# Kernel tuning notes

Hardware: AMD Instinct MI355X
Metric: run time of the kernel (lower is better)

Reference implementation:

```python
import jax, jax.numpy as jnp
import numpy as np

D_MODEL = 1024
NUM_HEADS = 16
DILATION_RATES = [2, 2, 2]
SEGMENT_SIZES = [64, 128, 256]
BATCH = 2
SEQ_LEN = 8192
N_LAYERS = len(SEGMENT_SIZES)


def setup_inputs() -> dict:
    key = jax.random.key(0)
    ks = jax.random.split(key, 5)
    d = D_MODEL
    scale = 1.0 / np.sqrt(d)
    x = jax.random.normal(ks[0], (BATCH, SEQ_LEN, d), dtype=jnp.float32)
    # Per-layer fused QKV + output projection params (stacked over layers)
    Wqkv = jax.random.normal(ks[1], (N_LAYERS, d, 3 * d), dtype=jnp.float32) * scale
    bqkv = jnp.zeros((N_LAYERS, 3 * d), dtype=jnp.float32)
    Wo = jax.random.normal(ks[2], (N_LAYERS, d, d), dtype=jnp.float32) * scale
    bo = jnp.zeros((N_LAYERS, d), dtype=jnp.float32)
    return {"x": x, "Wqkv": Wqkv, "bqkv": bqkv, "Wo": Wo, "bo": bo}


def _dilated_attention(x, Wqkv, bqkv, Wo, bo, seg, dr):
    # x: [B, S, D]. Segment, then dilate-stride within each segment.
    B, S, D = x.shape
    H = NUM_HEADS
    hd = D // H
    x4 = x.reshape(B, S // seg, seg, D)[:, :, ::dr, :]  # [B, N, s, D], s = seg//dr
    s = seg // dr
    N = S // seg
    qkv = jnp.einsum('bnsd,de->bnse', x4, Wqkv) + bqkv  # [B, N, s, 3D]
    q, k, v = jnp.split(qkv, 3, axis=-1)
    q = q.reshape(B, N, s, H, hd)
    k = k.reshape(B, N, s, H, hd)
    v = v.reshape(B, N, s, H, hd)
    # attention within each dilated segment
    scores = jnp.einsum('bnqhd,bnkhd->bnhqk', q, k) * (1.0 / np.sqrt(hd))
    attn = jax.nn.softmax(scores, axis=-1)
    o = jnp.einsum('bnhqk,bnkhd->bnqhd', attn, v).reshape(B, N, s, D)
    o = jnp.einsum('bnsd,de->bnse', o, Wo) + bo
    return o.reshape(B, N * s, D)  # [B, S/dr, D]


def reference(x, Wqkv, bqkv, Wo, bo):
    outs = []
    for i in range(N_LAYERS):
        outs.append(_dilated_attention(x, Wqkv[i], bqkv[i], Wo[i], bo[i],
                                       SEGMENT_SIZES[i], DILATION_RATES[i]))
    return jnp.stack(outs, axis=0).sum(axis=0)
```

## Files before the change

### kernel.cpp

```cpp
#include <hip/hip_runtime.h>
#include <hip/hip_bf16.h>
#include <stdint.h>

typedef unsigned short u16;
typedef short bf16x8 __attribute__((ext_vector_type(8)));
typedef u16   u16x8  __attribute__((ext_vector_type(8)));
typedef u16   u16x4  __attribute__((ext_vector_type(4)));
typedef float f32x4  __attribute__((ext_vector_type(4)));

__device__ inline u16 f2bf(float f) {
    uint32_t u = __builtin_bit_cast(uint32_t, f);
    uint32_t r = (u + 0x7FFFu + ((u >> 16) & 1u)) >> 16;
    return (u16)r;
}

__device__ inline void pin_barrier() {
    __builtin_amdgcn_sched_barrier(0);
    __builtin_amdgcn_s_barrier();
    __builtin_amdgcn_sched_barrier(0);
}

#define MFMA16(a, b, c) __builtin_amdgcn_mfma_f32_16x16x32_bf16((a), (b), (c), 0, 0, 0)

__global__ __launch_bounds__(256) void k_prep_xe(const float* __restrict__ x,
                                                 u16* __restrict__ xe) {
    int row = blockIdx.x;
    int b = row >> 12, tt = row & 4095;
    const float* src = x + ((size_t)b * 8192 + 2 * (size_t)tt) * 1024;
    float4 v = ((const float4*)src)[threadIdx.x];
    u16x4 o = { f2bf(v.x), f2bf(v.y), f2bf(v.z), f2bf(v.w) };
    *(u16x4*)(xe + (size_t)row * 1024 + threadIdx.x * 4) = o;
}

__global__ __launch_bounds__(256) void k_transpose_cast(
    const float* __restrict__ src, u16* __restrict__ dst,
    int srcCols, size_t srcLayerStride, int dstStride, int dstRowPer, int dstColPer) {
    int k0 = blockIdx.x * 64, e0 = blockIdx.y * 64, layer = blockIdx.z;
    const float* s = src + (size_t)layer * srcLayerStride;
    __shared__ u16 T[64][66];
    int t = threadIdx.x;
#pragma unroll
    for (int p = 0; p < 16; ++p) {
        int l = p * 256 + t;
        int kl = l >> 6, el = l & 63;
        T[kl][el] = f2bf(s[(size_t)(k0 + kl) * srcCols + e0 + el]);
    }
    __syncthreads();
    int rowBase = layer * dstRowPer + e0;
    int colBase = layer * dstColPer + k0;
#pragma unroll
    for (int p = 0; p < 16; ++p) {
        int l = p * 256 + t;
        int eo = l >> 6, ko = l & 63;
        dst[(size_t)(rowBase + eo) * dstStride + colBase + ko] = T[ko][eo];
    }
}

template <int BN, bool BF16OUT>
__global__ __launch_bounds__(512, 2) void k_gemm_rs(
    const u16* __restrict__ A, const u16* __restrict__ B, void* __restrict__ C,
    const float* __restrict__ bias0, const float* __restrict__ bias1,
    const float* __restrict__ bias2, int K, int lda, int ldb, int ldc,
    int gxmask, int gxshift) {
    constexpr int WN = BN / 64;
    constexpr int WM = 8 / WN;
    constexpr int MF = 256 / (WM * 16);
    constexpr int NF = 4;
    constexpr int NCA = 2;
    constexpr int NCB = (BN * 4) / 512;
    constexpr int NL = NCA + NCB;
    constexpr int SBUF = 16384 + BN * 64;

    __shared__ __align__(16) char smem[131072];
    const int tid = threadIdx.x, lane = tid & 63, wave = tid >> 6;
    const int wr = wave / WN, wc = wave % WN;

    const int nwg = gridDim.x, bid = blockIdx.x;
    const int cpx = nwg >> 3;
    const int swz = (bid & 7) * cpx + (bid >> 3);
    const int bx = swz & gxmask, by = swz >> gxshift;
    const int row0 = bx << 8;
    const int col0 = by * BN;

    const size_t lda2 = (size_t)lda * 2, ldb2 = (size_t)ldb * 2;
    const char* gA[NCA]; int wA[NCA];
    const char* gB[NCB]; int wB[NCB];
#pragma unroll
    for (int i = 0; i < NCA; ++i) {
        int c = tid + i * 512, row = c >> 2, cg = c & 3;
        gA[i] = (const char*)A + (size_t)(row0 + row) * lda2 + cg * 16;
        wA[i] = row * 64 + ((cg * 16) ^ (((row >> 3) & 1) << 5));
    }
#pragma unroll
    for (int i = 0; i < NCB; ++i) {
        int c = tid + i * 512, row = c >> 2, cg = c & 3;
        gB[i] = (const char*)B + (size_t)(col0 + row) * ldb2 + cg * 16;
        wB[i] = 16384 + row * 64 + ((cg * 16) ^ (((row >> 3) & 1) << 5));
    }

    const int lane_off = (lane & 15) * 64 +
                         (((lane >> 4) << 4) ^ (((lane >> 3) & 1) << 5));

    f32x4 acc[MF][NF] = {};
    const int nt = K >> 5;
    u16x8 uE[NL], uO[NL];

    auto LOADSET = [&](u16x8* u, int ts) {
#pragma unroll
        for (int i = 0; i < NCA; ++i)
            u[i] = *(const u16x8*)(gA[i] + (size_t)ts * 64);
#pragma unroll
        for (int i = 0; i < NCB; ++i)
            u[NCA + i] = *(const u16x8*)(gB[i] + (size_t)ts * 64);
    };
    auto WRITESET = [&](const u16x8* u, char* buf) {
#pragma unroll
        for (int i = 0; i < NCA; ++i) *(u16x8*)(buf + wA[i]) = u[i];
#pragma unroll
        for (int i = 0; i < NCB; ++i) *(u16x8*)(buf + wB[i]) = u[NCA + i];
    };
    auto WAIT_VM_NL = [&] {
        if constexpr (NL == 4) asm volatile("s_waitcnt vmcnt(4)" ::: "memory");
        else                   asm volatile("s_waitcnt vmcnt(3)" ::: "memory");
    };
    auto WAIT_LGKM_NL = [&] {
        if constexpr (NL == 4) asm volatile("s_waitcnt lgkmcnt(4)" ::: "memory");
        else                   asm volatile("s_waitcnt lgkmcnt(3)" ::: "memory");
    };
    auto TBODY = [&](const char* bufR, const u16x8* uW, char* bufW,
                     u16x8* uL, int tload) {
        const char* aRd = bufR + wr * (MF * 1024) + lane_off;
        const char* bRd = bufR + 16384 + wc * (NF * 1024) + lane_off;
        bf16x8 af[MF], bg[NF];
#pragma unroll
        for (int i = 0; i < MF; ++i) af[i] = *(const bf16x8*)(aRd + i * 1024);
#pragma unroll
        for (int i = 0; i < NF; ++i) bg[i] = *(const bf16x8*)(bRd + i * 1024);
        LOADSET(uL, tload);
        WAIT_VM_NL();
        WRITESET(uW, bufW);
        WAIT_LGKM_NL();
        __builtin_amdgcn_sched_barrier(0);
        __builtin_amdgcn_s_setprio(1);
#pragma unroll
        for (int m = 0; m < MF; ++m)
#pragma unroll
            for (int n = 0; n < NF; ++n)
                acc[m][n] = MFMA16(af[m], bg[n], acc[m][n]);
        __builtin_amdgcn_s_setprio(0);
        asm volatile("s_waitcnt lgkmcnt(0)" ::: "memory");
        pin_barrier();
    };

    LOADSET(uE, 0);
    LOADSET(uO, 1);
    WAIT_VM_NL();
    WRITESET(uE, smem);
    asm volatile("s_waitcnt lgkmcnt(0)" ::: "memory");
    pin_barrier();

    char* buf0 = smem;
    char* buf1 = smem + SBUF;
    for (int t = 0; t < nt; t += 2) {
        int l2 = (t + 2 < nt) ? t + 2 : nt - 1;
        int l3 = (t + 3 < nt) ? t + 3 : nt - 1;
        TBODY(buf0, uO, buf1, uE, l2);
        TBODY(buf1, uE, buf0, uO, l3);
    }

    {
        char* cst = smem;
        const int g4 = (lane >> 4) << 2, cl = lane & 15;
#pragma unroll
        for (int n = 0; n < NF; ++n) {
            int col = wc * (NF * 16) + n * 16 + cl;
            float bs = bias0[col0 + col];
            if (bias1) bs += bias1[col0 + col];
            if (bias2) bs += bias2[col0 + col];
#pragma unroll
            for (int m = 0; m < MF; ++m) {
#pragma unroll
                for (int r = 0; r < 4; ++r) {
                    int row = wr * (MF * 16) + m * 16 + g4 + r;
                    float v = acc[m][n][r] + bs;
                    if (BF16OUT) {
                        int scol = col ^ (((row >> 2) & 3) << 3);
                        *(u16*)(cst + row * 512 + scol * 2) = f2bf(v);
                    } else {
                        int scol = col ^ (((row >> 2) & 3) << 2);
                        *(float*)(cst + row * 512 + scol * 4) = v;
                    }
                }
            }
        }
        asm volatile("s_waitcnt lgkmcnt(0)" ::: "memory");
        pin_barrier();
        const int esz = BF16OUT ? 2 : 4;
#pragma unroll
        for (int it = 0; it < 16; ++it) {
            int id = it * 512 + tid;
            int row = id >> 5, c16 = id & 31;
            int sc16 = c16 ^ ((row >> 2) & 3);
            u16x8 v = *(const u16x8*)(cst + row * 512 + sc16 * 16);
            char* dst = (char*)C + ((size_t)(row0 + row) * ldc + col0) * esz + c16 * 16;
            *(u16x8*)dst = v;
        }
    }
}

template <int S>
__global__ __launch_bounds__(256) void k_attn(const u16* __restrict__ qkv,
                                              u16* __restrict__ ab, int layer) {
    constexpr int NCT = S / 16;
    constexpr int RPW = (S == 32) ? 1 : S / 64;
    constexpr int ACTIVE = (S == 32) ? 2 : 4;
    constexpr int KST = S / 32;
    constexpr int VSTRIDE = 2 * S;
    constexpr int VMASK = VSTRIDE / 16 - 1;

    __shared__ __align__(16) char KS[S * 128];
    __shared__ __align__(16) char VTS[64 * VSTRIDE];
    __shared__ __align__(16) char PS[S * VSTRIDE];

    const int per_b = (4096 / S) * 16;
    const int b = blockIdx.x / per_b;
    const int r0 = blockIdx.x % per_b;
    const int n = r0 >> 4, h = r0 & 15;
    const int token0 = b * 4096 + n * S;
    const int colQ = layer * 3072 + h * 64;
    const int tid = threadIdx.x, lane = tid & 63, wave = tid >> 6;

    constexpr int CHUNKS = S / 32;
#pragma unroll
    for (int c = 0; c < CHUNKS; ++c) {
        int lc = c * 256 + tid;
        int row = lc >> 3, off = (lc & 7) * 16;
        const char* base = (const char*)qkv + ((size_t)(token0 + row) * 9216 + colQ) * 2 + off;
        u16x8 kv = *(const u16x8*)(base + 1024 * 2);
        *(u16x8*)(KS + row * 128 + (off ^ ((row & 7) << 4))) = kv;
        u16x8 vv = *(const u16x8*)(base + 2048 * 2);
        int cb = off >> 1;
#pragma unroll
        for (int e = 0; e < 8; ++e) {
            int col = cb + e;
            *(u16*)(VTS + col * VSTRIDE + ((row * 2) ^ ((col & VMASK) << 4))) = vv[e];
        }
    }
    __syncthreads();

    f32x4 sacc[RPW][NCT] = {};
    if (wave < ACTIVE) {
#pragma unroll
        for (int rl = 0; rl < RPW; ++rl) {
            int rt = wave * RPW + rl;
#pragma unroll
            for (int ks2 = 0; ks2 < 2; ++ks2) {
                int qrow = token0 + rt * 16 + (lane & 15);
                int kbyte = ks2 * 64 + ((lane >> 4) << 4);
                bf16x8 aq = *(const bf16x8*)((const char*)qkv +
                              ((size_t)qrow * 9216 + colQ) * 2 + kbyte);
#pragma unroll
                for (int ct = 0; ct < NCT; ++ct) {
                    int krow = ct * 16 + (lane & 15);
                    bf16x8 bk = *(const bf16x8*)(KS + krow * 128 + (kbyte ^ ((krow & 7) << 4)));
                    sacc[rl][ct] = MFMA16(aq, bk, sacc[rl][ct]);
                }
            }
        }
#pragma unroll
        for (int rl = 0; rl < RPW; ++rl) {
            int rt = wave * RPW + rl;
#pragma unroll
            for (int r = 0; r < 4; ++r) {
                float vals[NCT];
                float m = -1e30f;
#pragma unroll
                for (int ct = 0; ct < NCT; ++ct) {
                    vals[ct] = sacc[rl][ct][r] * 0.125f;
                    m = fmaxf(m, vals[ct]);
                }
#pragma unroll
                for (int d = 1; d < 16; d <<= 1) m = fmaxf(m, __shfl_xor(m, d, 64));
                float sum = 0.f;
#pragma unroll
                for (int ct = 0; ct < NCT; ++ct) {
                    float p = exp2f((vals[ct] - m) * 1.44269504f);
                    vals[ct] = p;
                    sum += p;
                }
#pragma unroll
                for (int d = 1; d < 16; d <<= 1) sum += __shfl_xor(sum, d, 64);
                float inv = 1.0f / sum;
                int row = rt * 16 + ((lane >> 4) << 2) + r;
#pragma unroll
                for (int ct = 0; ct < NCT; ++ct) {
                    int col = ct * 16 + (lane & 15);
                    *(u16*)(PS + row * VSTRIDE + ((col * 2) ^ ((row & VMASK) << 4))) =
                        f2bf(vals[ct] * inv);
                }
            }
        }
    }
    __syncthreads();

    if (wave < ACTIVE) {
        const int colA = layer * 1024 + h * 64;
#pragma unroll
        for (int rl = 0; rl < RPW; ++rl) {
            int rt = wave * RPW + rl;
            f32x4 oacc[4] = {};
#pragma unroll
            for (int ks2 = 0; ks2 < KST; ++ks2) {
                int kbyte = ks2 * 64 + ((lane >> 4) << 4);
                int prow = rt * 16 + (lane & 15);
                bf16x8 ap = *(const bf16x8*)(PS + prow * VSTRIDE + (kbyte ^ ((prow & VMASK) << 4)));
#pragma unroll
                for (int ct = 0; ct < 4; ++ct) {
                    int vcol = ct * 16 + (lane & 15);
                    bf16x8 bv = *(const bf16x8*)(VTS + vcol * VSTRIDE + (kbyte ^ ((vcol & VMASK) << 4)));
                    oacc[ct] = MFMA16(ap, bv, oacc[ct]);
                }
            }
#pragma unroll
            for (int ct = 0; ct < 4; ++ct) {
#pragma unroll
                for (int r = 0; r < 4; ++r) {
                    int row = token0 + rt * 16 + ((lane >> 4) << 2) + r;
                    int col = colA + ct * 16 + (lane & 15);
                    ab[(size_t)row * 3072 + col] = f2bf(oacc[ct][r]);
                }
            }
        }
    }
}

extern "C" void kernel_launch(void* const* d_in, const int* in_sizes, int n_in,
                              void* d_out, int out_size, void* d_ws, size_t ws_size,
                              hipStream_t stream) {
    const float* x    = (const float*)d_in[0];
    const float* Wqkv = (const float*)d_in[1];
    const float* bqkv = (const float*)d_in[2];
    const float* Wo   = (const float*)d_in[3];
    const float* bo   = (const float*)d_in[4];

    char* ws = (char*)d_ws;
    u16* XE    = (u16*)(ws);
    u16* WQKVT = (u16*)(ws + 16777216);
    u16* WOT   = (u16*)(ws + 35651584);
    u16* QKVB  = (u16*)(ws + 41943040);
    u16* ABUF  = (u16*)(ws + 192937984);

    k_prep_xe<<<8192, 256, 0, stream>>>(x, XE);
    k_transpose_cast<<<dim3(16, 48, 3), 256, 0, stream>>>(
        Wqkv, WQKVT, 3072, (size_t)1024 * 3072, 1024, 3072, 0);
    k_transpose_cast<<<dim3(16, 16, 3), 256, 0, stream>>>(
        Wo, WOT, 1024, (size_t)1024 * 1024, 3072, 0, 1024);

    k_gemm_rs<256, true><<<dim3(1152), 512, 0, stream>>>(
        XE, WQKVT, QKVB, bqkv, nullptr, nullptr, 1024, 1024, 1024, 9216, 31, 5);

    k_attn<32><<<4096, 256, 0, stream>>>(QKVB, ABUF, 0);
    k_attn<64><<<2048, 256, 0, stream>>>(QKVB, ABUF, 1);
    k_attn<128><<<1024, 256, 0, stream>>>(QKVB, ABUF, 2);

    k_gemm_rs<128, false><<<dim3(256), 512, 0, stream>>>(
        ABUF, WOT, d_out, bo, bo + 1024, bo + 2048, 3072, 3072, 3072, 1024, 31, 5);
}
```

Measured before the change: 327.9 us.

## Use direct global-to-LDS loads with four-stage buffering in GEMM

Replaces the register-staged global loads and LDS writes in the GEMM with direct global_load_lds transfers. It moves from a two-buffer to a four-buffer LDS ring with three tiles prefetched, and changes the LDS swizzle to match the new write pattern. For the wide tile the MFMA work is split into two phases so B staging interleaves with compute. This aims to cut VGPR pressure and LDS write instructions and to hide global latency better, at the cost of more LDS and extra barriers per tile.

```diff
diff --git a/kernel.cpp b/kernel.cpp
--- a/kernel.cpp
+++ b/kernel.cpp
@@ -12,6 +12,11 @@
     uint32_t u = __builtin_bit_cast(uint32_t, f);
     uint32_t r = (u + 0x7FFFu + ((u >> 16) & 1u)) >> 16;
     return (u16)r;
+}
+
+__device__ inline void gload16(const void* g, void* l) {
+    __builtin_amdgcn_global_load_lds((const __attribute__((address_space(1))) void*)g,
+                                     (__attribute__((address_space(3))) void*)l, 16, 0, 0);
 }
 
 __device__ inline void pin_barrier() {
@@ -57,19 +62,18 @@
 }
 
 template <int BN, bool BF16OUT>
-__global__ __launch_bounds__(512, 2) void k_gemm_rs(
+__global__ __launch_bounds__(512, 2) void k_gemm3(
     const u16* __restrict__ A, const u16* __restrict__ B, void* __restrict__ C,
     const float* __restrict__ bias0, const float* __restrict__ bias1,
     const float* __restrict__ bias2, int K, int lda, int ldb, int ldc,
     int gxmask, int gxshift) {
     constexpr int WN = BN / 64;
     constexpr int WM = 8 / WN;
-    constexpr int MF = 256 / (WM * 16);
-    constexpr int NF = 4;
-    constexpr int NCA = 2;
-    constexpr int NCB = (BN * 4) / 512;
-    constexpr int NL = NCA + NCB;
-    constexpr int SBUF = 16384 + BN * 64;
+    constexpr int MFRAG = 16 / WM;
+    constexpr int PH = MFRAG / 4;
+    constexpr int NLB = BN / 128;
+    constexpr int NL = 2 + NLB;
+    constexpr int BUFSZ = 16384 + BN * 64;
 
     __shared__ __align__(16) char smem[131072];
     const int tid = threadIdx.x, lane = tid & 63, wave = tid >> 6;
@@ -79,109 +83,113 @@
     const int cpx = nwg >> 3;
     const int swz = (bid & 7) * cpx + (bid >> 3);
     const int bx = swz & gxmask, by = swz >> gxshift;
-    const int row0 = bx << 8;
-    const int col0 = by * BN;
+    const int row0 = bx << 8, col0 = by * BN;
 
     const size_t lda2 = (size_t)lda * 2, ldb2 = (size_t)ldb * 2;
-    const char* gA[NCA]; int wA[NCA];
-    const char* gB[NCB]; int wB[NCB];
-#pragma unroll
-    for (int i = 0; i < NCA; ++i) {
-        int c = tid + i * 512, row = c >> 2, cg = c & 3;
-        gA[i] = (const char*)A + (size_t)(row0 + row) * lda2 + cg * 16;
-        wA[i] = row * 64 + ((cg * 16) ^ (((row >> 3) & 1) << 5));
-    }
-#pragma unroll
-    for (int i = 0; i < NCB; ++i) {
-        int c = tid + i * 512, row = c >> 2, cg = c & 3;
-        gB[i] = (const char*)B + (size_t)(col0 + row) * ldb2 + cg * 16;
-        wB[i] = 16384 + row * 64 + ((cg * 16) ^ (((row >> 3) & 1) << 5));
-    }
+    const int r4 = tid >> 2;
+    const int cSw = ((lane & 3) ^ ((lane >> 3) & 3)) * 16;
+    const char* pA0 = (const char*)A + (size_t)(row0 + r4) * lda2 + cSw;
+    const char* pA1 = pA0 + (size_t)128 * lda2;
+    const char* pB0 = (const char*)B + (size_t)(col0 + r4) * ldb2 + cSw;
+    const char* pB1 = pB0 + (size_t)128 * ldb2;
+
+#define STAGE_A(sb, kof) do { \
+        gload16(pA0 + (kof), (sb) + wave * 1024); \
+        gload16(pA1 + (kof), (sb) + 8192 + wave * 1024); } while (0)
+#define STAGE_B(sb, kof) do { \
+        gload16(pB0 + (kof), (sb) + 16384 + wave * 1024); \
+        if constexpr (NLB == 2) gload16(pB1 + (kof), (sb) + 24576 + wave * 1024); \
+    } while (0)
+
+    auto WAIT_VM2NL = [] {
+        if constexpr (NL == 4) asm volatile("s_waitcnt vmcnt(8)" ::: "memory");
+        else                   asm volatile("s_waitcnt vmcnt(6)" ::: "memory");
+    };
 
     const int lane_off = (lane & 15) * 64 +
-                         (((lane >> 4) << 4) ^ (((lane >> 3) & 1) << 5));
-
-    f32x4 acc[MF][NF] = {};
+                         (((lane >> 4) << 4) ^ ((((lane & 15) >> 1) & 3) << 4));
+
+    f32x4 acc[8][4] = {};
     const int nt = K >> 5;
-    u16x8 uE[NL], uO[NL];
-
-    auto LOADSET = [&](u16x8* u, int ts) {
-#pragma unroll
-        for (int i = 0; i < NCA; ++i)
-            u[i] = *(const u16x8*)(gA[i] + (size_t)ts * 64);
-#pragma unroll
-        for (int i = 0; i < NCB; ++i)
-            u[NCA + i] = *(const u16x8*)(gB[i] + (size_t)ts * 64);
-    };
-    auto WRITESET = [&](const u16x8* u, char* buf) {
-#pragma unroll
-        for (int i = 0; i < NCA; ++i) *(u16x8*)(buf + wA[i]) = u[i];
-#pragma unroll
-        for (int i = 0; i < NCB; ++i) *(u16x8*)(buf + wB[i]) = u[NCA + i];
-    };
-    auto WAIT_VM_NL = [&] {
-        if constexpr (NL == 4) asm volatile("s_waitcnt vmcnt(4)" ::: "memory");
-        else                   asm volatile("s_waitcnt vmcnt(3)" ::: "memory");
-    };
-    auto WAIT_LGKM_NL = [&] {
-        if constexpr (NL == 4) asm volatile("s_waitcnt lgkmcnt(4)" ::: "memory");
-        else                   asm volatile("s_waitcnt lgkmcnt(3)" ::: "memory");
-    };
-    auto TBODY = [&](const char* bufR, const u16x8* uW, char* bufW,
-                     u16x8* uL, int tload) {
-        const char* aRd = bufR + wr * (MF * 1024) + lane_off;
-        const char* bRd = bufR + 16384 + wc * (NF * 1024) + lane_off;
-        bf16x8 af[MF], bg[NF];
-#pragma unroll
-        for (int i = 0; i < MF; ++i) af[i] = *(const bf16x8*)(aRd + i * 1024);
-#pragma unroll
-        for (int i = 0; i < NF; ++i) bg[i] = *(const bf16x8*)(bRd + i * 1024);
-        LOADSET(uL, tload);
-        WAIT_VM_NL();
-        WRITESET(uW, bufW);
-        WAIT_LGKM_NL();
-        __builtin_amdgcn_sched_barrier(0);
-        __builtin_amdgcn_s_setprio(1);
-#pragma unroll
-        for (int m = 0; m < MF; ++m)
-#pragma unroll
-            for (int n = 0; n < NF; ++n)
-                acc[m][n] = MFMA16(af[m], bg[n], acc[m][n]);
-        __builtin_amdgcn_s_setprio(0);
-        asm volatile("s_waitcnt lgkmcnt(0)" ::: "memory");
-        pin_barrier();
-    };
-
-    LOADSET(uE, 0);
-    LOADSET(uO, 1);
-    WAIT_VM_NL();
-    WRITESET(uE, smem);
-    asm volatile("s_waitcnt lgkmcnt(0)" ::: "memory");
+
+    char* const BUF0 = smem;
+    char* const BUF1 = smem + BUFSZ;
+    char* const BUF2 = smem + 2 * BUFSZ;
+    char* const BUF3 = smem + 3 * BUFSZ;
+
+    STAGE_A(BUF0, 0);   STAGE_B(BUF0, 0);
+    STAGE_A(BUF1, 64);  STAGE_B(BUF1, 64);
+    STAGE_A(BUF2, 128); STAGE_B(BUF2, 128);
+    __builtin_amdgcn_sched_barrier(0);
+    WAIT_VM2NL();
     pin_barrier();
 
-    char* buf0 = smem;
-    char* buf1 = smem + SBUF;
-    for (int t = 0; t < nt; t += 2) {
-        int l2 = (t + 2 < nt) ? t + 2 : nt - 1;
-        int l3 = (t + 3 < nt) ? t + 3 : nt - 1;
-        TBODY(buf0, uO, buf1, uE, l2);
-        TBODY(buf1, uE, buf0, uO, l3);
-    }
+#define TILE_BODY(qb, sb, ts) do { \
+        const char* aRd = (qb) + wr * (MFRAG * 1024) + lane_off; \
+        const char* bRd = (qb) + 16384 + wc * 4096 + lane_off; \
+        const size_t kof = (size_t)(ts) * 64; \
+        bf16x8 bg[4], af[4]; \
+        _Pragma("unroll") for (int n = 0; n < 4; ++n) \
+            bg[n] = *(const bf16x8*)(bRd + n * 1024); \
+        _Pragma("unroll") for (int m = 0; m < 4; ++m) \
+            af[m] = *(const bf16x8*)(aRd + m * 1024); \
+        STAGE_A(sb, kof); \
+        if constexpr (PH == 1) { STAGE_B(sb, kof); \
+            __builtin_amdgcn_sched_barrier(0); WAIT_VM2NL(); } \
+        pin_barrier(); \
+        __builtin_amdgcn_s_setprio(1); \
+        _Pragma("unroll") for (int m = 0; m < 4; ++m) \
+            _Pragma("unroll") for (int n = 0; n < 4; ++n) \
+                acc[m][n] = MFMA16(af[m], bg[n], acc[m][n]); \
+        __builtin_amdgcn_s_setprio(0); \
+        pin_barrier(); \
+        if constexpr (PH == 2) { \
+            bf16x8 af2[4]; \
+            _Pragma("unroll") for (int m = 0; m < 4; ++m) \
+                af2[m] = *(const bf16x8*)(aRd + (4 + m) * 1024); \
+            STAGE_B(sb, kof); \
+            __builtin_amdgcn_sched_barrier(0); WAIT_VM2NL(); \
+            pin_barrier(); \
+            __builtin_amdgcn_s_setprio(1); \
+            _Pragma("unroll") for (int m = 0; m < 4; ++m) \
+                _Pragma("unroll") for (int n = 0; n < 4; ++n) \
+                    acc[4 + m][n] = MFMA16(af2[m], bg[n], acc[4 + m][n]); \
+            __builtin_amdgcn_s_setprio(0); \
+            pin_barrier(); \
+        } \
+    } while (0)
+
+    for (int t = 0; t < nt; t += 4) {
+        int ts0 = (t + 3 < nt) ? t + 3 : nt - 1;
+        int ts1 = (t + 4 < nt) ? t + 4 : nt - 1;
+        int ts2 = (t + 5 < nt) ? t + 5 : nt - 1;
+        int ts3 = (t + 6 < nt) ? t + 6 : nt - 1;
+        TILE_BODY(BUF0, BUF3, ts0);
+        TILE_BODY(BUF1, BUF0, ts1);
+        TILE_BODY(BUF2, BUF1, ts2);
+        TILE_BODY(BUF3, BUF2, ts3);
+    }
+#undef TILE_BODY
+#undef STAGE_A
+#undef STAGE_B
 
     {
         char* cst = smem;
         const int g4 = (lane >> 4) << 2, cl = lane & 15;
-#pragma unroll
-        for (int n = 0; n < NF; ++n) {
-            int col = wc * (NF * 16) + n * 16 + cl;
+        __builtin_amdgcn_sched_barrier(0);
+        asm volatile("s_waitcnt vmcnt(0)" ::: "memory");
+        pin_barrier();
+#pragma unroll
+        for (int n = 0; n < 4; ++n) {
+            int col = wc * 64 + n * 16 + cl;
             float bs = bias0[col0 + col];
             if (bias1) bs += bias1[col0 + col];
             if (bias2) bs += bias2[col0 + col];
 #pragma unroll
-            for (int m = 0; m < MF; ++m) {
+            for (int m = 0; m < MFRAG; ++m) {
 #pragma unroll
                 for (int r = 0; r < 4; ++r) {
-                    int row = wr * (MF * 16) + m * 16 + g4 + r;
+                    int row = wr * (MFRAG * 16) + m * 16 + g4 + r;
                     float v = acc[m][n][r] + bs;
                     if (BF16OUT) {
                         int scol = col ^ (((row >> 2) & 3) << 3);
@@ -193,7 +201,6 @@
                 }
             }
         }
-        asm volatile("s_waitcnt lgkmcnt(0)" ::: "memory");
         pin_barrier();
         const int esz = BF16OUT ? 2 : 4;
 #pragma unroll
@@ -356,13 +363,13 @@
     k_transpose_cast<<<dim3(16, 16, 3), 256, 0, stream>>>(
         Wo, WOT, 1024, (size_t)1024 * 1024, 3072, 0, 1024);
 
-    k_gemm_rs<256, true><<<dim3(1152), 512, 0, stream>>>(
+    k_gemm3<256, true><<<dim3(1152), 512, 0, stream>>>(
         XE, WQKVT, QKVB, bqkv, nullptr, nullptr, 1024, 1024, 1024, 9216, 31, 5);
 
     k_attn<32><<<4096, 256, 0, stream>>>(QKVB, ABUF, 0);
     k_attn<64><<<2048, 256, 0, stream>>>(QKVB, ABUF, 1);
     k_attn<128><<<1024, 256, 0, stream>>>(QKVB, ABUF, 2);
 
-    k_gemm_rs<128, false><<<dim3(256), 512, 0, stream>>>(
+    k_gemm3<128, false><<<dim3(256), 512, 0, stream>>>(
         ABUF, WOT, d_out, bo, bo + 1024, bo + 2048, 3072, 3072, 3072, 1024, 31, 5);
 }
```

Measured after the change: 331.2 us. Within noise of the previous version (+1.0%).

## Rewrite GEMM main loop with direct global-to-LDS loads and BK=64 tiles

Applied to the files above, without the earlier changes.

The GEMM kernel stops staging tiles through registers (global load into VGPRs, then write to LDS). It now uses global_load_lds to copy 16-byte chunks straight into an XOR-swizzled shared-memory layout, and the K-step per iteration doubles to 64 with double buffering. MFMA groups are split into phases that overlap with the LDS fragment reads. The aim is to cut VGPR pressure, LDS write instructions and barrier count per unit of K. In exchange each iteration waits on vmcnt(0) for the full prefetch before its barrier, which may expose global-load latency.

```diff
diff --git a/kernel.cpp b/kernel.cpp
--- a/kernel.cpp
+++ b/kernel.cpp
@@ -12,6 +12,11 @@
     uint32_t u = __builtin_bit_cast(uint32_t, f);
     uint32_t r = (u + 0x7FFFu + ((u >> 16) & 1u)) >> 16;
     return (u16)r;
+}
+
+__device__ inline void gload16(const void* g, void* l) {
+    __builtin_amdgcn_global_load_lds((const __attribute__((address_space(1))) void*)g,
+                                     (__attribute__((address_space(3))) void*)l, 16, 0, 0);
 }
 
 __device__ inline void pin_barrier() {
@@ -57,19 +62,16 @@
 }
 
 template <int BN, bool BF16OUT>
-__global__ __launch_bounds__(512, 2) void k_gemm_rs(
+__global__ __launch_bounds__(512, 2) void k_gemm4(
     const u16* __restrict__ A, const u16* __restrict__ B, void* __restrict__ C,
     const float* __restrict__ bias0, const float* __restrict__ bias1,
     const float* __restrict__ bias2, int K, int lda, int ldb, int ldc,
     int gxmask, int gxshift) {
     constexpr int WN = BN / 64;
     constexpr int WM = 8 / WN;
-    constexpr int MF = 256 / (WM * 16);
-    constexpr int NF = 4;
-    constexpr int NCA = 2;
-    constexpr int NCB = (BN * 4) / 512;
-    constexpr int NL = NCA + NCB;
-    constexpr int SBUF = 16384 + BN * 64;
+    constexpr int MFRAG = 256 / (WM * 16);
+    constexpr int NB = BN / 64;
+    constexpr int BUFSZ = 32768 + BN * 128;
 
     __shared__ __align__(16) char smem[131072];
     const int tid = threadIdx.x, lane = tid & 63, wave = tid >> 6;
@@ -79,109 +81,135 @@
     const int cpx = nwg >> 3;
     const int swz = (bid & 7) * cpx + (bid >> 3);
     const int bx = swz & gxmask, by = swz >> gxshift;
-    const int row0 = bx << 8;
-    const int col0 = by * BN;
+    const int row0 = bx << 8, col0 = by * BN;
 
     const size_t lda2 = (size_t)lda * 2, ldb2 = (size_t)ldb * 2;
-    const char* gA[NCA]; int wA[NCA];
-    const char* gB[NCB]; int wB[NCB];
-#pragma unroll
-    for (int i = 0; i < NCA; ++i) {
-        int c = tid + i * 512, row = c >> 2, cg = c & 3;
-        gA[i] = (const char*)A + (size_t)(row0 + row) * lda2 + cg * 16;
-        wA[i] = row * 64 + ((cg * 16) ^ (((row >> 3) & 1) << 5));
-    }
-#pragma unroll
-    for (int i = 0; i < NCB; ++i) {
-        int c = tid + i * 512, row = c >> 2, cg = c & 3;
-        gB[i] = (const char*)B + (size_t)(col0 + row) * ldb2 + cg * 16;
-        wB[i] = 16384 + row * 64 + ((cg * 16) ^ (((row >> 3) & 1) << 5));
-    }
-
-    const int lane_off = (lane & 15) * 64 +
-                         (((lane >> 4) << 4) ^ (((lane >> 3) & 1) << 5));
-
-    f32x4 acc[MF][NF] = {};
-    const int nt = K >> 5;
-    u16x8 uE[NL], uO[NL];
-
-    auto LOADSET = [&](u16x8* u, int ts) {
-#pragma unroll
-        for (int i = 0; i < NCA; ++i)
-            u[i] = *(const u16x8*)(gA[i] + (size_t)ts * 64);
-#pragma unroll
-        for (int i = 0; i < NCB; ++i)
-            u[NCA + i] = *(const u16x8*)(gB[i] + (size_t)ts * 64);
-    };
-    auto WRITESET = [&](const u16x8* u, char* buf) {
-#pragma unroll
-        for (int i = 0; i < NCA; ++i) *(u16x8*)(buf + wA[i]) = u[i];
-#pragma unroll
-        for (int i = 0; i < NCB; ++i) *(u16x8*)(buf + wB[i]) = u[NCA + i];
-    };
-    auto WAIT_VM_NL = [&] {
-        if constexpr (NL == 4) asm volatile("s_waitcnt vmcnt(4)" ::: "memory");
-        else                   asm volatile("s_waitcnt vmcnt(3)" ::: "memory");
-    };
-    auto WAIT_LGKM_NL = [&] {
-        if constexpr (NL == 4) asm volatile("s_waitcnt lgkmcnt(4)" ::: "memory");
-        else                   asm volatile("s_waitcnt lgkmcnt(3)" ::: "memory");
-    };
-    auto TBODY = [&](const char* bufR, const u16x8* uW, char* bufW,
-                     u16x8* uL, int tload) {
-        const char* aRd = bufR + wr * (MF * 1024) + lane_off;
-        const char* bRd = bufR + 16384 + wc * (NF * 1024) + lane_off;
-        bf16x8 af[MF], bg[NF];
-#pragma unroll
-        for (int i = 0; i < MF; ++i) af[i] = *(const bf16x8*)(aRd + i * 1024);
-#pragma unroll
-        for (int i = 0; i < NF; ++i) bg[i] = *(const bf16x8*)(bRd + i * 1024);
-        LOADSET(uL, tload);
-        WAIT_VM_NL();
-        WRITESET(uW, bufW);
-        WAIT_LGKM_NL();
+    const char* pA0 = (const char*)A +
+        (size_t)(row0 + wave * 8 + (lane >> 3)) * lda2 + ((lane & 7) ^ (lane >> 3)) * 16;
+    const char* pB0 = (const char*)B +
+        (size_t)(col0 + wave * 8 + (lane >> 3)) * ldb2 + ((lane & 7) ^ (lane >> 3)) * 16;
+
+#define STA(i, sb, kof) gload16(pA0 + (size_t)(i) * 64 * lda2 + (kof), (sb) + ((i) * 8 + wave) * 1024)
+#define STB(i, sb, kof) gload16(pB0 + (size_t)(i) * 64 * ldb2 + (kof), (sb) + 32768 + ((i) * 8 + wave) * 1024)
+
+    const int la = lane & 15, lg = lane >> 4, l7 = lane & 7;
+    const int offK0 = la * 128 + ((lg ^ l7) << 4);
+    const int offK1 = la * 128 + (((4 + lg) ^ l7) << 4);
+
+    f32x4 acc[MFRAG][4] = {};
+    const int nt = K >> 6;
+
+    char* const BUF0 = smem;
+    char* const BUF1 = smem + BUFSZ;
+
+    {
+#pragma unroll
+        for (int i = 0; i < 4; ++i) STA(i, BUF0, 0);
+#pragma unroll
+        for (int i = 0; i < NB; ++i) STB(i, BUF0, 0);
         __builtin_amdgcn_sched_barrier(0);
+        asm volatile("s_waitcnt vmcnt(0)" ::: "memory");
+        pin_barrier();
+    }
+
+    for (int t = 0; t < nt; ++t) {
+        char* rq = (t & 1) ? BUF1 : BUF0;
+        char* sq = (t & 1) ? BUF0 : BUF1;
+        const bool st = (t + 1 < nt);
+        const size_t kof = (size_t)(t + 1) * 128;
+        const char* aB = rq + wr * (MFRAG * 2048);
+        const char* bB = rq + 32768 + wc * 8192;
+
+        bf16x8 af[4], ag[4], b0[4], b1[4];
+#pragma unroll
+        for (int n = 0; n < 4; ++n) b0[n] = *(const bf16x8*)(bB + n * 2048 + offK0);
+#pragma unroll
+        for (int m = 0; m < 4; ++m) af[m] = *(const bf16x8*)(aB + m * 2048 + offK0);
+        if (st) { STA(0, sq, kof); STA(1, sq, kof); }
+        if constexpr (MFRAG == 8) {
+#pragma unroll
+            for (int m = 0; m < 4; ++m)
+                ag[m] = *(const bf16x8*)(aB + 8192 + m * 2048 + offK0);
+        } else {
+#pragma unroll
+            for (int m = 0; m < 4; ++m)
+                ag[m] = *(const bf16x8*)(aB + m * 2048 + offK1);
+        }
+#pragma unroll
+        for (int n = 0; n < 4; ++n) b1[n] = *(const bf16x8*)(bB + n * 2048 + offK1);
+        if (st) {
+            STA(2, sq, kof); STA(3, sq, kof);
+#pragma unroll
+            for (int i = 0; i < NB; ++i) STB(i, sq, kof);
+        }
         __builtin_amdgcn_s_setprio(1);
 #pragma unroll
-        for (int m = 0; m < MF; ++m)
-#pragma unroll
-            for (int n = 0; n < NF; ++n)
-                acc[m][n] = MFMA16(af[m], bg[n], acc[m][n]);
+        for (int m = 0; m < 4; ++m)
+#pragma unroll
+            for (int n = 0; n < 4; ++n)
+                acc[m][n] = MFMA16(af[m], b0[n], acc[m][n]);
         __builtin_amdgcn_s_setprio(0);
-        asm volatile("s_waitcnt lgkmcnt(0)" ::: "memory");
+        __builtin_amdgcn_sched_barrier(0);
+
+        if constexpr (MFRAG == 8) {
+#pragma unroll
+            for (int m = 0; m < 4; ++m) af[m] = *(const bf16x8*)(aB + m * 2048 + offK1);
+            __builtin_amdgcn_s_setprio(1);
+#pragma unroll
+            for (int m = 0; m < 4; ++m)
+#pragma unroll
+                for (int n = 0; n < 4; ++n)
+                    acc[4 + m][n] = MFMA16(ag[m], b0[n], acc[4 + m][n]);
+            __builtin_amdgcn_s_setprio(0);
+            __builtin_amdgcn_sched_barrier(0);
+#pragma unroll
+            for (int m = 0; m < 4; ++m)
+                ag[m] = *(const bf16x8*)(aB + 8192 + m * 2048 + offK1);
+            __builtin_amdgcn_s_setprio(1);
+#pragma unroll
+            for (int m = 0; m < 4; ++m)
+#pragma unroll
+                for (int n = 0; n < 4; ++n)
+                    acc[m][n] = MFMA16(af[m], b1[n], acc[m][n]);
+            __builtin_amdgcn_s_setprio(0);
+            __builtin_amdgcn_sched_barrier(0);
+            __builtin_amdgcn_s_setprio(1);
+#pragma unroll
+            for (int m = 0; m < 4; ++m)
+#pragma unroll
+                for (int n = 0; n < 4; ++n)
+                    acc[4 + m][n] = MFMA16(ag[m], b1[n], acc[4 + m][n]);
+            __builtin_amdgcn_s_setprio(0);
+        } else {
+            __builtin_amdgcn_s_setprio(1);
+#pragma unroll
+            for (int m = 0; m < 4; ++m)
+#pragma unroll
+                for (int n = 0; n < 4; ++n)
+                    acc[m][n] = MFMA16(ag[m], b1[n], acc[m][n]);
+            __builtin_amdgcn_s_setprio(0);
+        }
+        __builtin_amdgcn_sched_barrier(0);
+        asm volatile("s_waitcnt vmcnt(0)" ::: "memory");
         pin_barrier();
-    };
-
-    LOADSET(uE, 0);
-    LOADSET(uO, 1);
-    WAIT_VM_NL();
-    WRITESET(uE, smem);
-    asm volatile("s_waitcnt lgkmcnt(0)" ::: "memory");
-    pin_barrier();
-
-    char* buf0 = smem;
-    char* buf1 = smem + SBUF;
-    for (int t = 0; t < nt; t += 2) {
-        int l2 = (t + 2 < nt) ? t + 2 : nt - 1;
-        int l3 = (t + 3 < nt) ? t + 3 : nt - 1;
-        TBODY(buf0, uO, buf1, uE, l2);
-        TBODY(buf1, uE, buf0, uO, l3);
-    }
+    }
+#undef STA
+#undef STB
 
     {
         char* cst = smem;
         const int g4 = (lane >> 4) << 2, cl = lane & 15;
 #pragma unroll
-        for (int n = 0; n < NF; ++n) {
-            int col = wc * (NF * 16) + n * 16 + cl;
+        for (int n = 0; n < 4; ++n) {
+            int col = wc * 64 + n * 16 + cl;
             float bs = bias0[col0 + col];
             if (bias1) bs += bias1[col0 + col];
             if (bias2) bs += bias2[col0 + col];
 #pragma unroll
-            for (int m = 0; m < MF; ++m) {
+            for (int m = 0; m < MFRAG; ++m) {
 #pragma unroll
                 for (int r = 0; r < 4; ++r) {
-                    int row = wr * (MF * 16) + m * 16 + g4 + r;
+                    int row = wr * (MFRAG * 16) + m * 16 + g4 + r;
                     float v = acc[m][n][r] + bs;
                     if (BF16OUT) {
                         int scol = col ^ (((row >> 2) & 3) << 3);
@@ -193,7 +221,6 @@
                 }
             }
         }
-        asm volatile("s_waitcnt lgkmcnt(0)" ::: "memory");
         pin_barrier();
         const int esz = BF16OUT ? 2 : 4;
 #pragma unroll
@@ -356,13 +383,13 @@
     k_transpose_cast<<<dim3(16, 16, 3), 256, 0, stream>>>(
         Wo, WOT, 1024, (size_t)1024 * 1024, 3072, 0, 1024);
 
-    k_gemm_rs<256, true><<<dim3(1152), 512, 0, stream>>>(
+    k_gemm4<256, true><<<dim3(1152), 512, 0, stream>>>(
         XE, WQKVT, QKVB, bqkv, nullptr, nullptr, 1024, 1024, 1024, 9216, 31, 5);
 
     k_attn<32><<<4096, 256, 0, stream>>>(QKVB, ABUF, 0);
     k_attn<64><<<2048, 256, 0, stream>>>(QKVB, ABUF, 1);
     k_attn<128><<<1024, 256, 0, stream>>>(QKVB, ABUF, 2);
 
-    k_gemm_rs<128, false><<<dim3(256), 512, 0, stream>>>(
+    k_gemm4<128, false><<<dim3(256), 512, 0, stream>>>(
         ABUF, WOT, d_out, bo, bo + 1024, bo + 2048, 3072, 3072, 3072, 1024, 31, 5);
 }
```

After: 323.6 us. Within noise of the previous version (-1.3%).
